# Performance work log

Hardware: AMD Instinct MI355X
Metric: run time of the kernel (lower is better)

## Reference

```python
import jax, jax.numpy as jnp
import numpy as np

N_NODES = 50000
N_EDGES = 800000
IN_CH = 128
HIDDEN = 64
LATENT = 64
OUT_CH = 128
N_GRAPHS = 500
NEG_SLOPE = 0.2


def _gat_layer(x, src, dst, W, a_src, a_dst, b, n_nodes):
    """PyG GATConv (heads=1, concat=True, add_self_loops=True, edge_dim=None)."""
    h = x @ W  # [N, F]
    loops = jnp.arange(n_nodes)
    s = jnp.concatenate([src, loops])  # source (j) of each edge incl. self loops
    d = jnp.concatenate([dst, loops])  # destination (i)
    score_src = h @ a_src  # [N]
    score_dst = h @ a_dst  # [N]
    alpha = jax.nn.leaky_relu(score_src[s] + score_dst[d], NEG_SLOPE)  # [E+N]
    # softmax grouped by destination node
    amax = jax.ops.segment_max(alpha, d, num_segments=n_nodes)
    e = jnp.exp(alpha - amax[d])
    denom = jax.ops.segment_sum(e, d, num_segments=n_nodes)
    coef = e / (denom[d] + 1e-16)
    out = jax.ops.segment_sum(h[s] * coef[:, None], d, num_segments=n_nodes)
    return out + b


def setup_inputs() -> dict:
    key = jax.random.key(0)
    ks = jax.random.split(key, 24)
    g = lambda k, shape, fan: jax.random.normal(k, shape, jnp.float32) * (1.0 / np.sqrt(fan))
    inp = {
        "x": jax.random.normal(ks[0], (N_NODES, IN_CH), jnp.float32),
        "edge_index": jax.random.randint(ks[1], (2, N_EDGES), 0, N_NODES, dtype=jnp.int64),
        "batch": jnp.sort(jax.random.randint(ks[2], (N_NODES,), 0, N_GRAPHS, dtype=jnp.int64)),
        "edge_attr": jax.random.normal(ks[3], (N_EDGES, 3), jnp.float32),
        # conv1 (GATConv in->hidden)
        "W1": g(ks[4], (IN_CH, HIDDEN), IN_CH),
        "a_src1": g(ks[5], (HIDDEN,), HIDDEN),
        "a_dst1": g(ks[6], (HIDDEN,), HIDDEN),
        "b1": jnp.zeros((HIDDEN,), jnp.float32),
        # conv2 (GATConv hidden->latent)
        "W2": g(ks[7], (HIDDEN, LATENT), HIDDEN),
        "a_src2": g(ks[8], (LATENT,), LATENT),
        "a_dst2": g(ks[9], (LATENT,), LATENT),
        "b2": jnp.zeros((LATENT,), jnp.float32),
        # encoder linear
        "lin_W": g(ks[10], (LATENT, LATENT), LATENT),
        "lin_b": jnp.zeros((LATENT,), jnp.float32),
        # decoder x_mlp
        "xm_W1": g(ks[11], (LATENT, HIDDEN), LATENT),
        "xm_b1": jnp.zeros((HIDDEN,), jnp.float32),
        "xm_W2": g(ks[12], (HIDDEN, OUT_CH), HIDDEN),
        "xm_b2": jnp.zeros((OUT_CH,), jnp.float32),
        # decoder edge_mlp
        "em_W1": g(ks[13], (LATENT, HIDDEN), LATENT),
        "em_b1": jnp.zeros((HIDDEN,), jnp.float32),
        "em_W2": g(ks[14], (HIDDEN, 3), HIDDEN),
        "em_b2": jnp.zeros((3,), jnp.float32),
    }
    return inp


def reference(x, edge_index, batch, edge_attr,
              W1, a_src1, a_dst1, b1,
              W2, a_src2, a_dst2, b2,
              lin_W, lin_b,
              xm_W1, xm_b1, xm_W2, xm_b2,
              em_W1, em_b1, em_W2, em_b2):
    src, dst = edge_index[0], edge_index[1]
    n = x.shape[0]
    # Encoder (eval mode: dropout is identity; edge_attr unused since edge_dim=None)
    h = _gat_layer(x, src, dst, W1, a_src1, a_dst1, b1, n)
    h = jax.nn.relu(h)
    z = _gat_layer(h, src, dst, W2, a_src2, a_dst2, b2, n)
    z = z @ lin_W + lin_b
    # global_mean_pool over batch ids
    sums = jax.ops.segment_sum(z, batch, num_segments=N_GRAPHS)
    counts = jax.ops.segment_sum(jnp.ones((n,), z.dtype), batch, num_segments=N_GRAPHS)
    graph_embedding = sums / jnp.maximum(counts, 1.0)[:, None]
    # MLP decoders
    x_hat = jax.nn.relu(z @ xm_W1 + xm_b1) @ xm_W2 + xm_b2
    e_hat = jax.nn.relu(z @ em_W1 + em_b1) @ em_W2 + em_b2
    return (x_hat, e_hat, z, graph_embedding)
```

## Files before the change

### kernel.cpp

```cpp
#include <hip/hip_runtime.h>
#include <hip/hip_bf16.h>
#include <cstring>

#define N_NODES 50000
#define N_EDGES 800000
#define IN_CH 128
#define NG 500
#define OUT_ELEMS 9782000
#define NBUCK 196
#define GEMMB 3125
#define DECB 3125

using bf16 = __hip_bfloat16;
typedef unsigned short u16;
typedef unsigned int u32;
typedef long long i64;
typedef unsigned long long u64;

__device__ __forceinline__ float b2f(bf16 v) { return __bfloat162float(v); }
__device__ __forceinline__ float tofl(float v) { return v; }
__device__ __forceinline__ float tofl(bf16 v) { return __bfloat162float(v); }
__device__ __forceinline__ float ldflt(const void* p, int i, int f32) {
  return f32 ? ((const float*)p)[i] : b2f(((const bf16*)p)[i]);
}
__device__ __forceinline__ int ldedge(const void* p, int i, int is64) {
  return is64 ? (int)((const i64*)p)[i] : ((const int*)p)[i];
}
__device__ __forceinline__ float sane(float v) {
  if (!isfinite(v)) return 0.f;
  return fminf(fmaxf(v, -65504.f), 65504.f);
}
__device__ __forceinline__ float lrelu(float x) { return x > 0.f ? x : 0.2f * x; }
__device__ __forceinline__ float bflo(u32 u) { return __uint_as_float(u << 16); }
__device__ __forceinline__ float bfhi(u32 u) { return __uint_as_float(u & 0xffff0000u); }

__device__ __forceinline__ float wsum(float v) {
#pragma unroll
  for (int o = 32; o > 0; o >>= 1) v += __shfl_xor(v, o, 64);
  return v;
}


__global__ void fillsig_kernel(float* __restrict__ out, int n, float v) {
  int i = blockIdx.x * 256 + threadIdx.x;
  if (i < n) out[i] = v;
}

__global__ __launch_bounds__(256) void prep_kernel(const u16* __restrict__ xb,
                                                   const int* __restrict__ ei32,
                                                   int* __restrict__ deg,
                                                   int* __restrict__ fl) {
  int bid = blockIdx.x, tid = threadIdx.x;
  if (bid < 196) {
    int i = bid * 256 + tid;
    if (i < N_NODES) deg[i] = 0;
    return;
  }
  __shared__ int c;
  if (tid == 0) c = 0;
  __syncthreads();
  int cnt = 0;
  if (bid == 196) {
#pragma unroll 4
    for (int k = 0; k < 32; ++k) {
      int i = tid + 256 * k;
      u16 u = xb[2 * i];
      int e = (u >> 7) & 0xFF;
      if (e != 0 && (e < 90 || e > 150)) ++cnt;
    }
  } else {
#pragma unroll 4
    for (int k = 0; k < 32; ++k) {
      int i = tid + 256 * k;
      if (ei32[2 * i + 1] == 0) ++cnt;
    }
  }
  atomicAdd(&c, cnt);
  __syncthreads();
  if (tid == 0) fl[bid == 196 ? 7 : 6] = c;
}

__global__ void hist_kernel(const void* __restrict__ ei, const int* __restrict__ fl,
                            int* __restrict__ deg) {
  int is64 = fl[6] > 4000;
  int e = blockIdx.x * 256 + threadIdx.x;
  if (e < N_EDGES) {
    unsigned d = (unsigned)ldedge(ei, N_EDGES + e, is64);
    if (d < N_NODES) atomicAdd(&deg[d], 1);
  }
}

__global__ __launch_bounds__(1024) void scan1_kernel(const int* __restrict__ deg,
                                                     int* __restrict__ offs,
                                                     int* __restrict__ part, int n) {
  __shared__ int sm[1024];
  int t = threadIdx.x;
  int idx = blockIdx.x * 1024 + t;
  int v = (idx < n) ? deg[idx] : 0;
  sm[t] = v;
  __syncthreads();
  for (int off = 1; off < 1024; off <<= 1) {
    int add = (t >= off) ? sm[t - off] : 0;
    __syncthreads();
    sm[t] += add;
    __syncthreads();
  }
  if (idx < n) offs[idx] = sm[t] - v;
  if (t == 1023) part[blockIdx.x] = sm[1023];
}

__global__ void scan3_kernel(int* __restrict__ offs, const int* __restrict__ part,
                             int* __restrict__ bcur, int n) {
  __shared__ int pbase;
  int b = blockIdx.x;
  int tid = threadIdx.x;
  if (tid == 0) {
    int bucket = b >> 2;
    int run = 0;
    for (int q = 0; q < bucket; ++q) run += part[q];
    pbase = run;
  }
  __syncthreads();
  int i = b * 256 + tid;
  if (i < n) {
    int v = offs[i] + pbase;
    offs[i] = v;
    if ((i & 255) == 0) bcur[i >> 8] = v;
  }
  if (i == 0) {
    int run = 0;
    for (int q = 0; q < 49; ++q) run += part[q];
    offs[n] = run;
  }
}

template <int FIN, typename FT>
__device__ void gemm16_compute(float (&xl)[16][FIN], const void* Wv, const void* asv,
                               const void* adv, bf16* __restrict__ h, float* __restrict__ ss,
                               float* __restrict__ sd, int rbase) {
  const FT* W = (const FT*)Wv;
  const FT* as_ = (const FT*)asv;
  const FT* ad_ = (const FT*)adv;
  int lane = threadIdx.x & 63, w = threadIdx.x >> 6;
  float a_s = tofl(as_[lane]), a_d = tofl(ad_[lane]);
  int r0 = w * 4;
  float acc0 = 0.f, acc1 = 0.f, acc2 = 0.f, acc3 = 0.f;
  for (int k = 0; k < FIN; ++k) {
    float wk = tofl(W[k * 64 + lane]);
    acc0 = fmaf(xl[r0 + 0][k], wk, acc0);
    acc1 = fmaf(xl[r0 + 1][k], wk, acc1);
    acc2 = fmaf(xl[r0 + 2][k], wk, acc2);
    acc3 = fmaf(xl[r0 + 3][k], wk, acc3);
  }
  float acc[4] = {sane(acc0), sane(acc1), sane(acc2), sane(acc3)};
#pragma unroll
  for (int j = 0; j < 4; ++j) {
    int g = rbase + r0 + j;
    h[g * 64 + lane] = __float2bfloat16(acc[j]);
    float vs = wsum(acc[j] * a_s);
    float vd = wsum(acc[j] * a_d);
    if (lane == 0) { ss[g] = sane(vs); sd[g] = sane(vd); }
  }
}

#define BCHUNK 4096
__global__ __launch_bounds__(256) void bucket_gemm_kernel(
    const void* __restrict__ ei, int* __restrict__ bcur, u64* __restrict__ tmp,
    const void* __restrict__ xin, const void* __restrict__ W, const void* __restrict__ asrc,
    const void* __restrict__ adst, const int* __restrict__ fl, bf16* __restrict__ h,
    float* __restrict__ ss, float* __restrict__ sd) {
  __shared__ int hist[NBUCK], run[NBUCK], gbase[NBUCK];
  __shared__ float xl[16][IN_CH];
  int bid = blockIdx.x, tid = threadIdx.x;
  int is64 = fl[6] > 4000;
  int wf = fl[7] > 2000;
  if (bid < NBUCK) {
    if (tid < NBUCK) { hist[tid] = 0; run[tid] = 0; }
    __syncthreads();
    int base = bid * BCHUNK;
#pragma unroll
    for (int k = 0; k < 16; ++k) {
      int e = base + k * 256 + tid;
      if (e < N_EDGES) {
        unsigned d = (unsigned)ldedge(ei, N_EDGES + e, is64);
        if (d < N_NODES) atomicAdd(&hist[d >> 8], 1);
      }
    }
    __syncthreads();
    if (tid < NBUCK) {
      int hh = hist[tid];
      gbase[tid] = hh ? atomicAdd(&bcur[tid], hh) : 0;
    }
    __syncthreads();
#pragma unroll
    for (int k = 0; k < 16; ++k) {
      int e = base + k * 256 + tid;
      if (e < N_EDGES) {
        unsigned d = (unsigned)ldedge(ei, N_EDGES + e, is64);
        if (d < N_NODES) {
          unsigned s = (unsigned)ldedge(ei, e, is64);
          if (s >= N_NODES) s = 0;
          int pos = gbase[d >> 8] + atomicAdd(&run[d >> 8], 1);
          tmp[pos] = ((u64)s << 32) | (u64)d;
        }
      }
    }
    return;
  }
  int rbase = (bid - NBUCK) * 16;
  for (int i = tid; i < 16 * IN_CH; i += 256) {
    int rr = i / IN_CH, cc = i % IN_CH;
    xl[rr][cc] = ldflt(xin, (rbase + rr) * IN_CH + cc, wf);
  }
  __syncthreads();
  if (wf)
    gemm16_compute<IN_CH, float>(xl, W, asrc, adst, h, ss, sd, rbase);
  else
    gemm16_compute<IN_CH, bf16>(xl, W, asrc, adst, h, ss, sd, rbase);
}

__global__ __launch_bounds__(1024) void scatter2_kernel(const u64* __restrict__ tmp,
                                                        const int* __restrict__ offs,
                                                        int* __restrict__ csr) {
  __shared__ int lcur[256];
  int b = blockIdx.x;
  int tid = threadIdx.x;
  if (tid < 256) lcur[tid] = 0;
  __syncthreads();
  int nodelo = b << 8;
  int beg = offs[nodelo];
  int end = offs[min(nodelo + 256, N_NODES)];
  for (int i = beg + tid; i < end; i += 1024) {
    u64 v = tmp[i];
    int d = (int)(v & 0xFFFFFFFFu);
    int s = (int)(v >> 32);
    unsigned li = (unsigned)(d - nodelo);
    if (li < 256) {
      int pos = offs[d] + atomicAdd(&lcur[li], 1);
      if ((unsigned)pos < N_EDGES) csr[pos] = s;
    }
  }
}

__device__ __forceinline__ float2 agg_node2(const bf16* __restrict__ h,
                                            const float* __restrict__ ss,
                                            const float* __restrict__ sd,
                                            const int* __restrict__ offs,
                                            const int* __restrict__ csr, int d, int lane) {
  int hl = lane & 31;
  int hbase = lane & 32;
  float sdd = sd[d];
  int beg = offs[d], end = offs[d + 1];
  beg = max(0, min(beg, N_EDGES));
  end = max(beg, min(end, N_EDGES));
  float wself = __expf(fminf(lrelu(ss[d] + sdd), 60.f));
  u32 uself = ((const u32*)h)[d * 32 + hl];
  float2 acc;
  acc.x = bflo(uself) * wself;
  acc.y = bfhi(uself) * wself;
  float dpart = (hl == 0) ? wself : 0.f;
  for (int cb = beg; cb < end; cb += 32) {
    int j = cb + hl;
    int s = 0;
    float wv = 0.f;
    if (j < end) {
      s = csr[j];
      s = ((unsigned)s < N_NODES) ? s : 0;
      wv = __expf(fminf(lrelu(ss[s] + sdd), 60.f));
    }
    dpart += wv;
    int cnt = min(32, end - cb);
    bool two = cnt > 16;
    u32 hv0[16], hv1[16];
#pragma unroll
    for (int q = 0; q < 16; ++q) {
      int sq = __shfl(s, hbase + q, 64);
      hv0[q] = ((const u32*)h)[sq * 32 + hl];
    }
    if (two) {
#pragma unroll
      for (int q = 0; q < 16; ++q) {
        int sq = __shfl(s, hbase + 16 + q, 64);
        hv1[q] = ((const u32*)h)[sq * 32 + hl];
      }
    }
#pragma unroll
    for (int q = 0; q < 16; ++q) {
      float wq = __shfl(wv, hbase + q, 64);
      acc.x = fmaf(bflo(hv0[q]), wq, acc.x);
      acc.y = fmaf(bfhi(hv0[q]), wq, acc.y);
    }
    if (two) {
#pragma unroll
      for (int q = 0; q < 16; ++q) {
        float wq = __shfl(wv, hbase + 16 + q, 64);
        acc.x = fmaf(bflo(hv1[q]), wq, acc.x);
        acc.y = fmaf(bfhi(hv1[q]), wq, acc.y);
      }
    }
  }
#pragma unroll
  for (int o = 16; o > 0; o >>= 1) dpart += __shfl_xor(dpart, o, 64);
  float den = dpart + 1e-16f;
  acc.x = acc.x / den;
  acc.y = acc.y / den;
  return acc;
}

template <typename FT>
__device__ void gemm2_compute(float (&xl)[8][64], int r0, const void* Wv, const void* asv,
                              const void* adv, bf16* __restrict__ h, float* __restrict__ ss,
                              float* __restrict__ sd, int rbase) {
  const FT* W = (const FT*)Wv;
  const FT* as_ = (const FT*)asv;
  const FT* ad_ = (const FT*)adv;
  int lane = threadIdx.x & 63;
  float a_s = tofl(as_[lane]), a_d = tofl(ad_[lane]);
  float acc0 = 0.f, acc1 = 0.f;
  for (int k = 0; k < 64; ++k) {
    float wk = tofl(W[k * 64 + lane]);
    acc0 = fmaf(xl[r0 + 0][k], wk, acc0);
    acc1 = fmaf(xl[r0 + 1][k], wk, acc1);
  }
  float acc[2] = {sane(acc0), sane(acc1)};
#pragma unroll
  for (int j = 0; j < 2; ++j) {
    int g = rbase + r0 + j;
    h[g * 64 + lane] = __float2bfloat16(acc[j]);
    float vs = wsum(acc[j] * a_s);
    float vd = wsum(acc[j] * a_d);
    if (lane == 0) { ss[g] = sane(vs); sd[g] = sane(vd); }
  }
}

template <typename FT>
__device__ void lin2_compute(float (&xl)[8][64], int r0, const void* Wv, const void* bv,
                             float* __restrict__ zio, int rbase) {
  const FT* W = (const FT*)Wv;
  const FT* b = (const FT*)bv;
  int lane = threadIdx.x & 63;
  float bl = tofl(b[lane]);
  float acc0 = bl, acc1 = bl;
  for (int k = 0; k < 64; ++k) {
    float wk = tofl(W[k * 64 + lane]);
    acc0 = fmaf(xl[r0 + 0][k], wk, acc0);
    acc1 = fmaf(xl[r0 + 1][k], wk, acc1);
  }
  float acc[2] = {sane(acc0), sane(acc1)};
#pragma unroll
  for (int j = 0; j < 2; ++j) zio[(rbase + r0 + j) * 64 + lane] = acc[j];
}

__global__ __launch_bounds__(256) void agg_gemm_kernel(
    const bf16* __restrict__ hL, const float* __restrict__ ssL, const float* __restrict__ sdL,
    const int* __restrict__ offs, const int* __restrict__ csr, const void* __restrict__ bias,
    const int* __restrict__ fl, const void* __restrict__ W2, const void* __restrict__ as2,
    const void* __restrict__ ad2, bf16* __restrict__ hOut, float* __restrict__ ssOut,
    float* __restrict__ sdOut) {
  __shared__ float o1l[8][64];
  int wf = fl[7] > 2000;
  int lane = threadIdx.x & 63, w = threadIdx.x >> 6;
  int hl = lane & 31, half = lane >> 5;
  int rbase = blockIdx.x * 8;
  int d = rbase + 2 * w + half;
  float2 r = agg_node2(hL, ssL, sdL, offs, csr, d, lane);
  float blx = ldflt(bias, 2 * hl, wf), bly = ldflt(bias, 2 * hl + 1, wf);
  o1l[2 * w + half][2 * hl] = sane(fmaxf(r.x + blx, 0.f));
  o1l[2 * w + half][2 * hl + 1] = sane(fmaxf(r.y + bly, 0.f));
  __syncthreads();
  if (wf)
    gemm2_compute<float>(o1l, 2 * w, W2, as2, ad2, hOut, ssOut, sdOut, rbase);
  else
    gemm2_compute<bf16>(o1l, 2 * w, W2, as2, ad2, hOut, ssOut, sdOut, rbase);
}

__global__ __launch_bounds__(256) void agg_lin_kernel(
    const bf16* __restrict__ hL, const float* __restrict__ ssL, const float* __restrict__ sdL,
    const int* __restrict__ offs, const int* __restrict__ csr, const void* __restrict__ bias,
    const int* __restrict__ fl, const void* __restrict__ linW, const void* __restrict__ linb,
    float* __restrict__ zreg) {
  __shared__ float o2l[8][64];
  int wf = fl[7] > 2000;
  int lane = threadIdx.x & 63, w = threadIdx.x >> 6;
  int hl = lane & 31, half = lane >> 5;
  int rbase = blockIdx.x * 8;
  int d = rbase + 2 * w + half;
  float2 r = agg_node2(hL, ssL, sdL, offs, csr, d, lane);
  float blx = ldflt(bias, 2 * hl, wf), bly = ldflt(bias, 2 * hl + 1, wf);
  o2l[2 * w + half][2 * hl] = sane(r.x + blx);
  o2l[2 * w + half][2 * hl + 1] = sane(r.y + bly);
  __syncthreads();
  if (wf)
    lin2_compute<float>(o2l, 2 * w, linW, linb, zreg, rbase);
  else
    lin2_compute<bf16>(o2l, 2 * w, linW, linb, zreg, rbase);
}

template <typename FT>
__device__ void dec16_compute(float (&zl)[16][64], float (&t1x)[16][64], float (&t1e)[16][65],
                              float (&W2l)[192], const void* xW1v, const void* xb1v,
                              const void* xW2v, const void* xb2v, const void* eW1v,
                              const void* eb1v, const void* eb2v, float* __restrict__ xout,
                              float* __restrict__ eout, int rbase) {
  const FT* xW1 = (const FT*)xW1v;
  const FT* xb1 = (const FT*)xb1v;
  const FT* xW2 = (const FT*)xW2v;
  const FT* xb2 = (const FT*)xb2v;
  const FT* eW1 = (const FT*)eW1v;
  const FT* eb1 = (const FT*)eb1v;
  const FT* eb2 = (const FT*)eb2v;
  int lane = threadIdx.x & 63, w = threadIdx.x >> 6;
  int r0 = w * 4;
  {
    float bx = tofl(xb1[lane]), be = tofl(eb1[lane]);
    float x0 = bx, x1 = bx, x2 = bx, x3 = bx;
    float e0 = be, e1 = be, e2 = be, e3 = be;
    for (int k = 0; k < 64; ++k) {
      float z0 = zl[r0 + 0][k], z1 = zl[r0 + 1][k];
      float z2 = zl[r0 + 2][k], z3 = zl[r0 + 3][k];
      float wx = tofl(xW1[k * 64 + lane]);
      float we = tofl(eW1[k * 64 + lane]);
      x0 = fmaf(z0, wx, x0);
      x1 = fmaf(z1, wx, x1);
      x2 = fmaf(z2, wx, x2);
      x3 = fmaf(z3, wx, x3);
      e0 = fmaf(z0, we, e0);
      e1 = fmaf(z1, we, e1);
      e2 = fmaf(z2, we, e2);
      e3 = fmaf(z3, we, e3);
    }
    t1x[r0 + 0][lane] = fmaxf(x0, 0.f);
    t1x[r0 + 1][lane] = fmaxf(x1, 0.f);
    t1x[r0 + 2][lane] = fmaxf(x2, 0.f);
    t1x[r0 + 3][lane] = fmaxf(x3, 0.f);
    t1e[r0 + 0][lane] = fmaxf(e0, 0.f);
    t1e[r0 + 1][lane] = fmaxf(e1, 0.f);
    t1e[r0 + 2][lane] = fmaxf(e2, 0.f);
    t1e[r0 + 3][lane] = fmaxf(e3, 0.f);
  }
  {
    float b2a = tofl(xb2[lane]), b2b = tofl(xb2[64 + lane]);
    float a0[4] = {b2a, b2a, b2a, b2a};
    float a1[4] = {b2b, b2b, b2b, b2b};
    for (int k = 0; k < 64; ++k) {
      float wa = tofl(xW2[k * 128 + lane]);
      float wb = tofl(xW2[k * 128 + 64 + lane]);
#pragma unroll
      for (int j = 0; j < 4; ++j) {
        float tv = t1x[r0 + j][k];
        a0[j] = fmaf(tv, wa, a0[j]);
        a1[j] = fmaf(tv, wb, a1[j]);
      }
    }
#pragma unroll
    for (int j = 0; j < 4; ++j) {
      int g = rbase + r0 + j;
      xout[g * 128 + lane] = sane(a0[j]);
      xout[g * 128 + 64 + lane] = sane(a1[j]);
    }
  }
  {
    int j = lane >> 4, c = lane & 15;
    if (c < 3) {
      int row = r0 + j;
      float acc = tofl(eb2[c]);
#pragma unroll 4
      for (int k = 0; k < 64; ++k) acc = fmaf(t1e[row][k], W2l[k * 3 + c], acc);
      eout[(rbase + row) * 3 + c] = sane(acc);
    }
  }
}

__global__ __launch_bounds__(256) void dec_pool_kernel(
    const float* __restrict__ z, const void* __restrict__ xmW1, const void* __restrict__ xmb1,
    const void* __restrict__ xmW2, const void* __restrict__ xmb2, const void* __restrict__ emW1,
    const void* __restrict__ emb1, const void* __restrict__ emW2, const void* __restrict__ emb2,
    const void* __restrict__ batch, const int* __restrict__ fl, float* __restrict__ xout,
    float* __restrict__ eout, float* __restrict__ emb) {
  __shared__ float zl[16][64];
  __shared__ float t1x[16][64];
  __shared__ float t1e[16][65];
  __shared__ float W2l[192];
  int tid = threadIdx.x;
  if (blockIdx.x < NG) {
    float(&sm)[4][64] = *reinterpret_cast<float(*)[4][64]>(&zl[0][0]);
    int* bounds = (int*)&t1x[0][0];
    int g = blockIdx.x;
    int lane = tid & 63, w = tid >> 6;
    int is64 = fl[6] > 4000;
    if (tid < 2) {
      int target = g + tid;
      int lo = 0, hi = N_NODES;
      while (lo < hi) {
        int mid = (lo + hi) >> 1;
        if (ldedge(batch, mid, is64) < target) lo = mid + 1; else hi = mid;
      }
      bounds[tid] = lo;
    }
    __syncthreads();
    int beg = bounds[0], end = bounds[1];
    float acc = 0.f;
    for (int r = beg + w; r < end; r += 4) acc += z[r * 64 + lane];
    sm[w][lane] = acc;
    __syncthreads();
    if (w == 0) {
      float v = sm[0][lane] + sm[1][lane] + sm[2][lane] + sm[3][lane];
      float cnt = (float)max(end - beg, 1);
      emb[g * 64 + lane] = sane(v / cnt);
    }
    return;
  }
  int wf = fl[7] > 2000;
  int rbase = (blockIdx.x - NG) * 16;
  for (int i = tid; i < 1024; i += 256) zl[i >> 6][i & 63] = z[rbase * 64 + i];
  if (tid < 192) W2l[tid] = wf ? ((const float*)emW2)[tid] : b2f(((const bf16*)emW2)[tid]);
  __syncthreads();
  if (wf)
    dec16_compute<float>(zl, t1x, t1e, W2l, xmW1, xmb1, xmW2, xmb2, emW1, emb1, emb2,
                         xout, eout, rbase);
  else
    dec16_compute<bf16>(zl, t1x, t1e, W2l, xmW1, xmb1, xmW2, xmb2, emW1, emb1, emb2,
                        xout, eout, rbase);
}

extern "C" void kernel_launch(void* const* d_in, const int* in_sizes, int n_in,
                              void* d_out, int out_size, void* d_ws, size_t ws_size,
                              hipStream_t stream) {
  float* outf = (float*)d_out;
  if (out_size != OUT_ELEMS) {
    float sig = 2048.0f + fminf((float)out_size * 1e-4f, 999.f);
    fillsig_kernel<<<(out_size + 255) / 256, 256, 0, stream>>>(outf, out_size, sig);
    return;
  }
  if (n_in < 22 || in_sizes[0] != N_NODES * IN_CH || in_sizes[1] != 2 * N_EDGES) {
    fillsig_kernel<<<(out_size + 255) / 256, 256, 0, stream>>>(outf, out_size, 5000.f);
    return;
  }

  const void* x = d_in[0];
  const void* ei = d_in[1];
  const void* batch = d_in[2];
  const void* W1 = d_in[4];
  const void* as1 = d_in[5];
  const void* ad1 = d_in[6];
  const void* b1 = d_in[7];
  const void* W2 = d_in[8];
  const void* as2 = d_in[9];
  const void* ad2 = d_in[10];
  const void* b2 = d_in[11];
  const void* linW = d_in[12];
  const void* linb = d_in[13];
  const void* xmW1 = d_in[14];
  const void* xmb1 = d_in[15];
  const void* xmW2 = d_in[16];
  const void* xmb2 = d_in[17];
  const void* emW1 = d_in[18];
  const void* emb1 = d_in[19];
  const void* emW2 = d_in[20];
  const void* emb2 = d_in[21];

  float* xhat = outf;
  float* ehat = outf + 6400000;
  float* zreg = outf + 6550000;
  float* emb = outf + 9750000;

  bool usews = ws_size >= (size_t)17100000;
  char* base = usews ? (char*)d_ws : (char*)d_out;
  int* deg = (int*)(base + 0);
  int* bcur = (int*)(base + 200000);
  int* offs = (int*)(base + 400000);
  int* part = (int*)(base + 600016);
  int* flags = (int*)(base + 600272);
  float* ssb = (float*)(base + 600448);
  float* sdb = (float*)(base + 800448);
  int* csr = (int*)(base + 1000448);
  bf16* hbuf = (bf16*)(base + 4200448);
  u64* tmp = (u64*)(base + 10600448);
  float* ss2 = (float*)(base + 0);
  float* sd2 = (float*)(base + 200000);
  bf16* hbuf2 = (bf16*)(base + 10600448);

  int err = 0, idx = 0;
  (void)hipGetLastError();
#define CK()                                                                       \
  do {                                                                             \
    ++idx;                                                                         \
    hipError_t e_ = hipGetLastError();                                             \
    if (e_ != hipSuccess && err == 0) err = 8192 + idx * 256 + ((int)e_ & 3) * 64; \
  } while (0)

  prep_kernel<<<198, 256, 0, stream>>>((const u16*)x, (const int*)ei, deg, flags); CK();
  hist_kernel<<<N_EDGES / 256, 256, 0, stream>>>(ei, flags, deg); CK();
  scan1_kernel<<<49, 1024, 0, stream>>>(deg, offs, part, N_NODES); CK();
  scan3_kernel<<<(N_NODES + 255) / 256, 256, 0, stream>>>(offs, part, bcur, N_NODES); CK();
  bucket_gemm_kernel<<<NBUCK + GEMMB, 256, 0, stream>>>(
      ei, bcur, tmp, x, W1, as1, ad1, flags, hbuf, ssb, sdb); CK();
  scatter2_kernel<<<NBUCK, 1024, 0, stream>>>(tmp, offs, csr); CK();
  agg_gemm_kernel<<<N_NODES / 8, 256, 0, stream>>>(hbuf, ssb, sdb, offs, csr, b1, flags,
                                                   W2, as2, ad2, hbuf2, ss2, sd2); CK();
  agg_lin_kernel<<<N_NODES / 8, 256, 0, stream>>>(hbuf2, ss2, sd2, offs, csr, b2, flags,
                                                  linW, linb, zreg); CK();
  dec_pool_kernel<<<NG + DECB, 256, 0, stream>>>(zreg, xmW1, xmb1, xmW2, xmb2,
                                                 emW1, emb1, emW2, emb2, batch, flags,
                                                 xhat, ehat, emb); CK();
#undef CK

  if (err != 0) {
    static float s_sent;
    s_sent = (float)err;
    (void)hipMemcpyAsync(d_out, &s_sent, 4, hipMemcpyHostToDevice, stream);
  }
}
```

Baseline: 334.0 us.

## Replace per-node degree histogram and scans with bucket-level counts and local CSR offsets

```diff
diff --git a/kernel.cpp b/kernel.cpp
--- a/kernel.cpp
+++ b/kernel.cpp
@@ -46,21 +46,40 @@
   if (i < n) out[i] = v;
 }
 
-__global__ __launch_bounds__(256) void prep_kernel(const u16* __restrict__ xb,
-                                                   const int* __restrict__ ei32,
-                                                   int* __restrict__ deg,
-                                                   int* __restrict__ fl) {
+#define BCHUNK 4096
+
+__global__ __launch_bounds__(256) void hist196_kernel(const void* __restrict__ ei,
+                                                      const u16* __restrict__ xb,
+                                                      int* __restrict__ bpart,
+                                                      int* __restrict__ fl) {
   int bid = blockIdx.x, tid = threadIdx.x;
-  if (bid < 196) {
-    int i = bid * 256 + tid;
-    if (i < N_NODES) deg[i] = 0;
+  __shared__ int cs;
+  __shared__ int hist[NBUCK];
+  if (bid < NBUCK) {
+    if (tid == 0) cs = 0;
+    if (tid < NBUCK) hist[tid] = 0;
+    __syncthreads();
+    const int* e32 = (const int*)ei;
+    atomicAdd(&cs, (e32[2 * tid + 1] == 0) ? 1 : 0);
+    __syncthreads();
+    int is64 = cs > 128;
+    int base = bid * BCHUNK;
+#pragma unroll
+    for (int k = 0; k < 16; ++k) {
+      int e = base + k * 256 + tid;
+      if (e < N_EDGES) {
+        unsigned d = (unsigned)ldedge(ei, N_EDGES + e, is64);
+        if (d < N_NODES) atomicAdd(&hist[d >> 8], 1);
+      }
+    }
+    __syncthreads();
+    if (tid < NBUCK) bpart[bid * 256 + tid] = hist[tid];
     return;
   }
-  __shared__ int c;
-  if (tid == 0) c = 0;
+  if (tid == 0) cs = 0;
   __syncthreads();
   int cnt = 0;
-  if (bid == 196) {
+  if (bid == NBUCK) {
 #pragma unroll 4
     for (int k = 0; k < 32; ++k) {
       int i = tid + 256 * k;
@@ -69,68 +88,43 @@
       if (e != 0 && (e < 90 || e > 150)) ++cnt;
     }
   } else {
+    const int* e32 = (const int*)ei;
 #pragma unroll 4
     for (int k = 0; k < 32; ++k) {
       int i = tid + 256 * k;
-      if (ei32[2 * i + 1] == 0) ++cnt;
-    }
-  }
-  atomicAdd(&c, cnt);
-  __syncthreads();
-  if (tid == 0) fl[bid == 196 ? 7 : 6] = c;
-}
-
-__global__ void hist_kernel(const void* __restrict__ ei, const int* __restrict__ fl,
-                            int* __restrict__ deg) {
-  int is64 = fl[6] > 4000;
-  int e = blockIdx.x * 256 + threadIdx.x;
-  if (e < N_EDGES) {
-    unsigned d = (unsigned)ldedge(ei, N_EDGES + e, is64);
-    if (d < N_NODES) atomicAdd(&deg[d], 1);
-  }
-}
-
-__global__ __launch_bounds__(1024) void scan1_kernel(const int* __restrict__ deg,
-                                                     int* __restrict__ offs,
-                                                     int* __restrict__ part, int n) {
-  __shared__ int sm[1024];
+      if (e32[2 * i + 1] == 0) ++cnt;
+    }
+  }
+  atomicAdd(&cs, cnt);
+  __syncthreads();
+  if (tid == 0) fl[bid == NBUCK ? 7 : 6] = cs;
+}
+
+__global__ __launch_bounds__(256) void scan196_kernel(const int* __restrict__ bpart,
+                                                      int* __restrict__ bcur,
+                                                      int* __restrict__ bstart,
+                                                      int* __restrict__ offs) {
+  __shared__ int sm[256];
   int t = threadIdx.x;
-  int idx = blockIdx.x * 1024 + t;
-  int v = (idx < n) ? deg[idx] : 0;
-  sm[t] = v;
-  __syncthreads();
-  for (int off = 1; off < 1024; off <<= 1) {
+  int sum = 0;
+  if (t < NBUCK)
+    for (int b = 0; b < NBUCK; ++b) sum += bpart[b * 256 + t];
+  sm[t] = (t < NBUCK) ? sum : 0;
+  __syncthreads();
+  for (int off = 1; off < 256; off <<= 1) {
     int add = (t >= off) ? sm[t - off] : 0;
     __syncthreads();
     sm[t] += add;
     __syncthreads();
   }
-  if (idx < n) offs[idx] = sm[t] - v;
-  if (t == 1023) part[blockIdx.x] = sm[1023];
-}
-
-__global__ void scan3_kernel(int* __restrict__ offs, const int* __restrict__ part,
-                             int* __restrict__ bcur, int n) {
-  __shared__ int pbase;
-  int b = blockIdx.x;
-  int tid = threadIdx.x;
-  if (tid == 0) {
-    int bucket = b >> 2;
-    int run = 0;
-    for (int q = 0; q < bucket; ++q) run += part[q];
-    pbase = run;
-  }
-  __syncthreads();
-  int i = b * 256 + tid;
-  if (i < n) {
-    int v = offs[i] + pbase;
-    offs[i] = v;
-    if ((i & 255) == 0) bcur[i >> 8] = v;
-  }
-  if (i == 0) {
-    int run = 0;
-    for (int q = 0; q < 49; ++q) run += part[q];
-    offs[n] = run;
+  if (t < NBUCK) {
+    int start = sm[t] - sum;
+    bcur[t] = start;
+    bstart[t] = start;
+  }
+  if (t == 255) {
+    bstart[NBUCK] = sm[255];
+    offs[N_NODES] = sm[255];
   }
 }
 
@@ -163,7 +157,6 @@
   }
 }
 
-#define BCHUNK 4096
 __global__ __launch_bounds__(256) void bucket_gemm_kernel(
     const void* __restrict__ ei, int* __restrict__ bcur, u64* __restrict__ tmp,
     const void* __restrict__ xin, const void* __restrict__ W, const void* __restrict__ asrc,
@@ -201,7 +194,7 @@
           unsigned s = (unsigned)ldedge(ei, e, is64);
           if (s >= N_NODES) s = 0;
           int pos = gbase[d >> 8] + atomicAdd(&run[d >> 8], 1);
-          tmp[pos] = ((u64)s << 32) | (u64)d;
+          if ((unsigned)pos < N_EDGES) tmp[pos] = ((u64)s << 32) | (u64)d;
         }
       }
     }
@@ -219,24 +212,47 @@
     gemm16_compute<IN_CH, bf16>(xl, W, asrc, adst, h, ss, sd, rbase);
 }
 
-__global__ __launch_bounds__(1024) void scatter2_kernel(const u64* __restrict__ tmp,
-                                                        const int* __restrict__ offs,
-                                                        int* __restrict__ csr) {
-  __shared__ int lcur[256];
+__global__ __launch_bounds__(1024) void scatter2b_kernel(const u64* __restrict__ tmp,
+                                                         const int* __restrict__ bstart,
+                                                         int* __restrict__ offs,
+                                                         int* __restrict__ csr) {
+  __shared__ int lcnt[256], lex[256], lcur[256];
   int b = blockIdx.x;
   int tid = threadIdx.x;
-  if (tid < 256) lcur[tid] = 0;
+  if (tid < 256) { lcnt[tid] = 0; lcur[tid] = 0; }
   __syncthreads();
   int nodelo = b << 8;
-  int beg = offs[nodelo];
-  int end = offs[min(nodelo + 256, N_NODES)];
+  int beg = bstart[b], end = bstart[b + 1];
+  beg = max(0, min(beg, N_EDGES));
+  end = max(beg, min(end, N_EDGES));
+  for (int i = beg + tid; i < end; i += 1024) {
+    int d = (int)(tmp[i] & 0xFFFFFFFFu);
+    unsigned li = (unsigned)(d - nodelo);
+    if (li < 256) atomicAdd(&lcnt[li], 1);
+  }
+  __syncthreads();
+  if (tid < 256) lex[tid] = lcnt[tid];
+  __syncthreads();
+  for (int off = 1; off < 256; off <<= 1) {
+    int add = (tid < 256 && tid >= off) ? lex[tid - off] : 0;
+    __syncthreads();
+    if (tid < 256) lex[tid] += add;
+    __syncthreads();
+  }
+  if (tid < 256) {
+    int ex = lex[tid] - lcnt[tid];
+    lex[tid] = ex;
+    int node = nodelo + tid;
+    if (node < N_NODES) offs[node] = beg + ex;
+  }
+  __syncthreads();
   for (int i = beg + tid; i < end; i += 1024) {
     u64 v = tmp[i];
     int d = (int)(v & 0xFFFFFFFFu);
     int s = (int)(v >> 32);
     unsigned li = (unsigned)(d - nodelo);
     if (li < 256) {
-      int pos = offs[d] + atomicAdd(&lcur[li], 1);
+      int pos = beg + lex[li] + atomicAdd(&lcur[li], 1);
       if ((unsigned)pos < N_EDGES) csr[pos] = s;
     }
   }
@@ -270,32 +286,18 @@
     }
     dpart += wv;
     int cnt = min(32, end - cb);
-    bool two = cnt > 16;
-    u32 hv0[16], hv1[16];
-#pragma unroll
-    for (int q = 0; q < 16; ++q) {
-      int sq = __shfl(s, hbase + q, 64);
-      hv0[q] = ((const u32*)h)[sq * 32 + hl];
-    }
-    if (two) {
+    for (int t0 = 0; t0 < cnt; t0 += 16) {
+      u32 hv[16];
 #pragma unroll
       for (int q = 0; q < 16; ++q) {
-        int sq = __shfl(s, hbase + 16 + q, 64);
-        hv1[q] = ((const u32*)h)[sq * 32 + hl];
+        int sq = __shfl(s, hbase + t0 + q, 64);
+        hv[q] = ((const u32*)h)[sq * 32 + hl];
       }
-    }
-#pragma unroll
-    for (int q = 0; q < 16; ++q) {
-      float wq = __shfl(wv, hbase + q, 64);
-      acc.x = fmaf(bflo(hv0[q]), wq, acc.x);
-      acc.y = fmaf(bfhi(hv0[q]), wq, acc.y);
-    }
-    if (two) {
 #pragma unroll
       for (int q = 0; q < 16; ++q) {
-        float wq = __shfl(wv, hbase + 16 + q, 64);
-        acc.x = fmaf(bflo(hv1[q]), wq, acc.x);
-        acc.y = fmaf(bfhi(hv1[q]), wq, acc.y);
+        float wq = __shfl(wv, hbase + t0 + q, 64);
+        acc.x = fmaf(bflo(hv[q]), wq, acc.x);
+        acc.y = fmaf(bfhi(hv[q]), wq, acc.y);
       }
     }
   }
@@ -566,19 +568,19 @@
 
   bool usews = ws_size >= (size_t)17100000;
   char* base = usews ? (char*)d_ws : (char*)d_out;
-  int* deg = (int*)(base + 0);
-  int* bcur = (int*)(base + 200000);
+  int* bpart = (int*)(base + 0);
   int* offs = (int*)(base + 400000);
-  int* part = (int*)(base + 600016);
-  int* flags = (int*)(base + 600272);
-  float* ssb = (float*)(base + 600448);
-  float* sdb = (float*)(base + 800448);
-  int* csr = (int*)(base + 1000448);
-  bf16* hbuf = (bf16*)(base + 4200448);
-  u64* tmp = (u64*)(base + 10600448);
+  int* bcur = (int*)(base + 600016);
+  int* bstart = (int*)(base + 600816);
+  int* flags = (int*)(base + 601616);
+  float* ssb = (float*)(base + 601728);
+  float* sdb = (float*)(base + 801728);
+  int* csr = (int*)(base + 1001728);
+  bf16* hbuf = (bf16*)(base + 4201728);
+  u64* tmp = (u64*)(base + 10601728);
   float* ss2 = (float*)(base + 0);
   float* sd2 = (float*)(base + 200000);
-  bf16* hbuf2 = (bf16*)(base + 10600448);
+  bf16* hbuf2 = (bf16*)(base + 10601728);
 
   int err = 0, idx = 0;
   (void)hipGetLastError();
@@ -589,13 +591,11 @@
     if (e_ != hipSuccess && err == 0) err = 8192 + idx * 256 + ((int)e_ & 3) * 64; \
   } while (0)
 
-  prep_kernel<<<198, 256, 0, stream>>>((const u16*)x, (const int*)ei, deg, flags); CK();
-  hist_kernel<<<N_EDGES / 256, 256, 0, stream>>>(ei, flags, deg); CK();
-  scan1_kernel<<<49, 1024, 0, stream>>>(deg, offs, part, N_NODES); CK();
-  scan3_kernel<<<(N_NODES + 255) / 256, 256, 0, stream>>>(offs, part, bcur, N_NODES); CK();
+  hist196_kernel<<<NBUCK + 2, 256, 0, stream>>>(ei, (const u16*)x, bpart, flags); CK();
+  scan196_kernel<<<1, 256, 0, stream>>>(bpart, bcur, bstart, offs); CK();
   bucket_gemm_kernel<<<NBUCK + GEMMB, 256, 0, stream>>>(
       ei, bcur, tmp, x, W1, as1, ad1, flags, hbuf, ssb, sdb); CK();
-  scatter2_kernel<<<NBUCK, 1024, 0, stream>>>(tmp, offs, csr); CK();
+  scatter2b_kernel<<<NBUCK, 1024, 0, stream>>>(tmp, bstart, offs, csr); CK();
   agg_gemm_kernel<<<N_NODES / 8, 256, 0, stream>>>(hbuf, ssb, sdb, offs, csr, b1, flags,
                                                    W2, as2, ad2, hbuf2, ss2, sd2); CK();
   agg_lin_kernel<<<N_NODES / 8, 256, 0, stream>>>(hbuf2, ss2, sd2, offs, csr, b2, flags,
```

Result: faster. 305.7 us (-8.5%).
